# Performance work log

Hardware: AMD Instinct MI355X
Metric: run time of the kernel (lower is better)

## Reference

```python
import jax, jax.numpy as jnp
import numpy as np

SIGMA = 16.0


def setup_inputs() -> dict:
    key = jax.random.key(0)
    k1, k2, k3 = jax.random.split(key, 3)
    B, T, D = 8, 2048, 1024
    x = jax.random.normal(k1, (B, T, D), dtype=jnp.float32)
    posv = jax.random.randint(k2, (B, T), 0, 64, dtype=jnp.int32)
    posh = jax.random.randint(k3, (B, T), 0, 64, dtype=jnp.int32)
    return {"x": x, "posv": posv, "posh": posh}


def reference(x, posv, posh):
    # pos: [B, T, 2] float, as in torch.stack([posv, posh], -1).float()
    pos = jnp.stack([posv, posh], axis=-1).astype(jnp.float32)
    # pairwise squared distances: [B, T, T]
    diff = pos[:, :, None, :] - pos[:, None, :, :]
    dist_sq = jnp.sum(diff * diff, axis=-1)
    kernel = jnp.exp(-dist_sq / (2.0 * SIGMA * SIGMA))
    kernel = kernel / jnp.sum(kernel, axis=-1, keepdims=True)
    # dropout is identity in eval mode
    return jnp.einsum("bts,bsd->btd", kernel, x)
```

## Files before the change

### kernel.cpp

```cpp
#include <hip/hip_runtime.h>
#include <hip/hip_bf16.h>

#define NB 8
#define NT 2048
#define ND 1024
#define CAP 2048

typedef unsigned short ushort_t;
using short8 = __attribute__((ext_vector_type(8))) short;
using f32x4  = __attribute__((ext_vector_type(4))) float;

__device__ __forceinline__ ushort_t f2bf(float f) {
    __hip_bfloat16 h = __float2bfloat16(f);
    return *reinterpret_cast<ushort_t*>(&h);
}
__device__ __forceinline__ float bf2f(ushort_t u) {
    unsigned int v = ((unsigned int)u) << 16;
    return __int_as_float((int)v);
}


#define OFF_G2     256
#define OFF_AFH    768
#define OFF_AFL    8960
#define OFF_CNTV   17152
#define OFF_CNTH   19200
#define OFF_INVDEN 21248
#define OFF_GOFF   152320
#define OFF_TOKV   160512
#define OFF_TOKH   4354816
#define OFF_TOKV2  8549120
#define OFF_B1     12743424
#define B1_SLAB    ((size_t)64 * 64 * 1024 * 2)

__global__ __launch_bounds__(256) void k1_bucket(
    const int* __restrict__ posv, const int* __restrict__ posh,
    int* __restrict__ tokv, int* __restrict__ tokh,
    int* __restrict__ cntv, int* __restrict__ cnth,
    float* __restrict__ gbase, ushort_t* __restrict__ AfH,
    ushort_t* __restrict__ AfL)
{
    int b    = blockIdx.x >> 5;
    int blk  = blockIdx.x & 31;
    int wave = threadIdx.x >> 6;
    int lane = threadIdx.x & 63;

    if (blockIdx.x == 0) {
        if (threadIdx.x < 192) {
            int k = (int)threadIdx.x - 64;
            float v = 0.0f;
            if (k >= 0 && k < 127) {
                int r = k - 63;
                v = expf(-(float)(r * r) * (1.0f / 512.0f));
            }
            gbase[threadIdx.x] = v;
        }
#pragma unroll
        for (int p = 0; p < 16; p++) {
            int pos = (p << 8) + (int)threadIdx.x;
            int i   = pos & 7;
            int ln  = (pos >> 3) & 63;
            int ks  = (pos >> 9) & 1;
            int w   = pos >> 10;
            int q   = (w << 4) + (ln & 15);
            int k   = (ks << 5) + ((i >> 2) << 4) + ((ln >> 4) << 2) + (i & 3);
            int dlt = q - k;
            float g = expf(-(float)(dlt * dlt) * (1.0f / 512.0f));
            ushort_t hi = f2bf(g);
            AfH[pos] = hi;
            AfL[pos] = f2bf(g - bf2f(hi));
        }
    }

    int task   = blk * 4 + wave;
    int bucket = task & 63;
    int use_ph = task >> 6;
    const int* pos  = use_ph ? posh : posv;
    const int* opos = use_ph ? posv : posh;
    int* tok = (use_ph ? tokh : tokv) + ((size_t)(b * 64 + bucket)) * CAP;
    int* cnt = use_ph ? cnth : cntv;

    int vals[32];
#pragma unroll
    for (int k = 0; k < 32; k++) vals[k] = pos[b * NT + k * 64 + lane];

    unsigned long long lmask = (1ull << lane) - 1ull;
    int cursor = 0;
#pragma unroll 4
    for (int k = 0; k < 32; k++) {
        bool hit = (vals[k] == bucket);
        unsigned long long m = __ballot(hit);
        if (hit) {
            int t = k * 64 + lane;
            tok[cursor + __popcll(m & lmask)] = t | (opos[b * NT + t] << 16);
        }
        cursor += (int)__popcll(m);
    }
    if (lane == 0) cnt[b * 64 + bucket] = cursor;
}

__global__ __launch_bounds__(256) void k1b_group(
    const int* __restrict__ tokv, const int* __restrict__ cntv,
    int* __restrict__ tokv2, int4* __restrict__ goff)
{
    int bucket = blockIdx.x * 4 + (threadIdx.x >> 6);
    int lane   = threadIdx.x & 63;
    int n = cntv[bucket];
    const int* src = tokv + (size_t)bucket * CAP;
    int* dst = tokv2 + (size_t)bucket * CAP;
    unsigned long long lmask = (1ull << lane) - 1ull;

    int cnt0 = 0, cnt1 = 0, cnt2 = 0, cnt3 = 0;
    for (int base = 0; base < n; base += 64) {
        bool valid = base + lane < n;
        int pk = valid ? src[base + lane] : 0;
        int grp = (pk >> 20) & 3;
        cnt0 += (int)__popcll(__ballot(valid && grp == 0));
        cnt1 += (int)__popcll(__ballot(valid && grp == 1));
        cnt2 += (int)__popcll(__ballot(valid && grp == 2));
        cnt3 += (int)__popcll(__ballot(valid && grp == 3));
    }
    int s1 = cnt0, s2 = cnt0 + cnt1, s3 = cnt0 + cnt1 + cnt2;
    if (lane == 0) goff[bucket] = make_int4(0, s1, s2, s3);

    int c0 = 0, c1 = s1, c2 = s2, c3 = s3;
    for (int base = 0; base < n; base += 64) {
        bool valid = base + lane < n;
        int pk = valid ? src[base + lane] : 0;
        int grp = (pk >> 20) & 3;
        unsigned long long m0 = __ballot(valid && grp == 0);
        unsigned long long m1 = __ballot(valid && grp == 1);
        unsigned long long m2 = __ballot(valid && grp == 2);
        unsigned long long m3 = __ballot(valid && grp == 3);
        if (valid) {
            int p;
            if      (grp == 0) p = c0 + (int)__popcll(m0 & lmask);
            else if (grp == 1) p = c1 + (int)__popcll(m1 & lmask);
            else if (grp == 2) p = c2 + (int)__popcll(m2 & lmask);
            else               p = c3 + (int)__popcll(m3 & lmask);
            dst[p] = pk;
        }
        c0 += (int)__popcll(m0); c1 += (int)__popcll(m1);
        c2 += (int)__popcll(m2); c3 += (int)__popcll(m3);
    }
}

__global__ __launch_bounds__(256) void kden(
    const int* __restrict__ posv, const int* __restrict__ posh,
    const float* __restrict__ G2f, float* __restrict__ invden, int b0)
{
    int b   = b0 + (blockIdx.x >> 3);
    int phg = blockIdx.x & 7;
    int tid = threadIdx.x;

    __shared__ int   hist[64][64];
    __shared__ float g2s[128];
    __shared__ float tmp[64][8];

#pragma unroll
    for (int k = 0; k < 16; k++) ((int*)hist)[tid + (k << 8)] = 0;
    if (tid < 128) g2s[tid] = G2f[tid];
    __syncthreads();
#pragma unroll
    for (int k = 0; k < 8; k++) {
        int t = (k << 8) + tid;
        atomicAdd(&hist[posv[b * NT + t]][posh[b * NT + t]], 1);
    }
    __syncthreads();
#pragma unroll
    for (int c = 0; c < 2; c++) {
        int cell = (c << 8) + tid;
        int j    = cell >> 3;
        int phl  = cell & 7;
        int ph   = (phg << 3) + phl;
        float s = 0.f;
        for (int k = 0; k < 64; k++)
            s += (float)hist[j][k] * g2s[63 + k - ph];
        tmp[j][phl] = s;
    }
    __syncthreads();
#pragma unroll
    for (int c = 0; c < 2; c++) {
        int cell = (c << 8) + tid;
        int pv   = cell >> 3;
        int phl  = cell & 7;
        int ph   = (phg << 3) + phl;
        float s = 0.f;
        for (int j = 0; j < 64; j++)
            s += g2s[63 + j - pv] * tmp[j][phl];
        invden[(b * 64 + pv) * 64 + ph] = 1.0f / s;
    }
}

__device__ __forceinline__ short8 ldsBfrag(const ushort_t* rowp, int ks, int g4) {
    const ushort_t* p = rowp + (ks << 5) + g4;
    uint2 lo = *(const uint2*)(p);
    uint2 hi = *(const uint2*)(p + 16);
    uint4 pk; pk.x = lo.x; pk.y = lo.y; pk.z = hi.x; pk.w = hi.y;
    return __builtin_bit_cast(short8, pk);
}

__global__ __launch_bounds__(256) void k2_convh(
    const float* __restrict__ x,
    const int* __restrict__ tokv2, const int* __restrict__ cntv,
    const int4* __restrict__ goff,
    const ushort_t* __restrict__ AfH, const ushort_t* __restrict__ AfL,
    ushort_t* __restrict__ B1, int b0)
{
    int pv   = blockIdx.x & 63;
    int dc   = (blockIdx.x >> 6) & 15;
    int b    = b0 + (blockIdx.x >> 10);
    int tid  = threadIdx.x;
    int lane = tid & 63;
    int w    = tid >> 6;
    int d0   = dc << 6;

    __shared__ float ldsf[64 * 65];
    float    (*S)[65]   = (float(*)[65])ldsf;
    ushort_t (*S16)[68] = (ushort_t(*)[68])ldsf;

    int bucket = (b << 6) + pv;
    int n = cntv[bucket];
    const int* toks = tokv2 + (size_t)bucket * CAP;
    const float* xb = x + (((size_t)b * NT) << 10) + d0 + lane;

    int4 go = goff[bucket];
    int gs = (w == 0) ? go.x : (w == 1) ? go.y : (w == 2) ? go.z : go.w;
    int ge = (w == 3) ? n   : (w == 0) ? go.y : (w == 1) ? go.z : go.w;

    int wn0 = ge - gs; if (wn0 < 0) wn0 = 0; if (wn0 > 64) wn0 = 64;
    int m0  = wn0 > 8 ? 8 : wn0;
    int pkv = (wn0 > 0) ? toks[gs + lane] : 0;
    int pk0[8]; float xv0[8];
#pragma unroll
    for (int j = 0; j < 8; j++) pk0[j] = __builtin_amdgcn_readlane(pkv, j);
#pragma unroll
    for (int j = 0; j < 8; j++)
        if (j < m0) xv0[j] = xb[(size_t)(pk0[j] & 0xffff) << 10];

#pragma unroll
    for (int k = 0; k < 17; k++) {
        int idx = (k << 8) + tid;
        if (idx < 64 * 65) ldsf[idx] = 0.f;
    }
    __syncthreads();

#pragma unroll
    for (int j = 0; j < 8; j++)
        if (j < m0) S[lane][pk0[j] >> 16] += xv0[j];

    for (int i = 8; i < wn0; i += 8) {
        int m = wn0 - i; if (m > 8) m = 8;
        int pk[8]; float xv[8];
#pragma unroll
        for (int j = 0; j < 8; j++) pk[j] = __builtin_amdgcn_readlane(pkv, i + j);
#pragma unroll
        for (int j = 0; j < 8; j++)
            if (j < m) xv[j] = xb[(size_t)(pk[j] & 0xffff) << 10];
#pragma unroll
        for (int j = 0; j < 8; j++)
            if (j < m) S[lane][pk[j] >> 16] += xv[j];
    }
    for (int win = gs + 64; win < ge; win += 64) {
        int wn = ge - win; if (wn > 64) wn = 64;
        int pkw = toks[win + lane];
        for (int i = 0; i < wn; i += 8) {
            int m = wn - i; if (m > 8) m = 8;
            int pk[8]; float xv[8];
#pragma unroll
            for (int j = 0; j < 8; j++) pk[j] = __builtin_amdgcn_readlane(pkw, i + j);
#pragma unroll
            for (int j = 0; j < 8; j++)
                if (j < m) xv[j] = xb[(size_t)(pk[j] & 0xffff) << 10];
#pragma unroll
            for (int j = 0; j < 8; j++)
                if (j < m) S[lane][pk[j] >> 16] += xv[j];
        }
    }
    __syncthreads();

    {
        int r  = tid & 63;
        int c0 = (tid >> 6) << 4;
        float vals[16];
#pragma unroll
        for (int c = 0; c < 16; c++) vals[c] = S[r][c0 + c];
        __syncthreads();
#pragma unroll
        for (int c = 0; c < 16; c++) S16[r][c0 + c] = f2bf(vals[c]);
    }
    __syncthreads();

    short8 ahi[2], alo[2];
#pragma unroll
    for (int ks = 0; ks < 2; ks++) {
        int idx = ((((w << 1) + ks) << 6) + lane) << 3;
        ahi[ks] = *(const short8*)(AfH + idx);
        alo[ks] = *(const short8*)(AfL + idx);
    }
    int g4 = (lane >> 4) << 2;
    int qbase = (w << 4) + g4;

    f32x4 accs[4];
#pragma unroll
    for (int nt = 0; nt < 4; nt++) {
        const ushort_t* rowp = &S16[(nt << 4) + (lane & 15)][0];
        f32x4 acc = {0.f, 0.f, 0.f, 0.f};
#pragma unroll
        for (int ks = 0; ks < 2; ks++) {
            short8 bf = ldsBfrag(rowp, ks, g4);
            acc = __builtin_amdgcn_mfma_f32_16x16x32_bf16(ahi[ks], bf, acc, 0, 0, 0);
            acc = __builtin_amdgcn_mfma_f32_16x16x32_bf16(alo[ks], bf, acc, 0, 0, 0);
        }
        accs[nt] = acc;
    }
    __syncthreads();

#pragma unroll
    for (int nt = 0; nt < 4; nt++)
#pragma unroll
        for (int reg = 0; reg < 4; reg++)
            S16[qbase + reg][(nt << 4) + (lane & 15)] = f2bf(accs[nt][reg]);
    __syncthreads();

    ushort_t* B1p = B1 + (((size_t)(b - b0)) << 22) + (((size_t)pv) << 10) + d0;
#pragma unroll
    for (int pass = 0; pass < 2; pass++) {
        int row = (pass << 5) + (tid >> 3);
        int col = (tid & 7) << 3;
        uint4 v = *(const uint4*)(&S16[row][col]);
        *reinterpret_cast<uint4*>(B1p + ((size_t)row << 16) + col) = v;
    }
}

__global__ __launch_bounds__(256) void k3_convv(
    const int* __restrict__ tokh, const int* __restrict__ cnth,
    const ushort_t* __restrict__ AfH, const ushort_t* __restrict__ AfL,
    const ushort_t* __restrict__ B1, const float* __restrict__ invden,
    float* __restrict__ out, int b0)
{
    int ph   = blockIdx.x & 63;
    int dc   = (blockIdx.x >> 6) & 15;
    int b    = b0 + (blockIdx.x >> 10);
    int tid  = threadIdx.x;
    int lane = tid & 63;
    int w    = tid >> 6;
    int d0   = dc << 6;

    int n = cnth[(b << 6) + ph];
    if (n == 0) return;

    __shared__ float ldsf[64 * 65];
    ushort_t (*u16)[68] = (ushort_t(*)[68])ldsf;
    float    (*y)[65]   = (float(*)[65])ldsf;

    const ushort_t* B1b = B1 + (((size_t)(b - b0)) << 22) + (((size_t)ph) << 16)
                        + d0 + lane;
#pragma unroll
    for (int it = 0; it < 16; it++) {
        int j = (w << 4) + it;
        u16[lane][j] = B1b[(size_t)j << 10];
    }
    __syncthreads();

    short8 ahi[2], alo[2];
#pragma unroll
    for (int ks = 0; ks < 2; ks++) {
        int idx = ((((w << 1) + ks) << 6) + lane) << 3;
        ahi[ks] = *(const short8*)(AfH + idx);
        alo[ks] = *(const short8*)(AfL + idx);
    }
    int g4 = (lane >> 4) << 2;
    int qbase = (w << 4) + g4;

    f32x4 accs[4];
#pragma unroll
    for (int nt = 0; nt < 4; nt++) {
        const ushort_t* rowp = &u16[(nt << 4) + (lane & 15)][0];
        f32x4 acc = {0.f, 0.f, 0.f, 0.f};
#pragma unroll
        for (int ks = 0; ks < 2; ks++) {
            short8 bf = ldsBfrag(rowp, ks, g4);
            acc = __builtin_amdgcn_mfma_f32_16x16x32_bf16(ahi[ks], bf, acc, 0, 0, 0);
            acc = __builtin_amdgcn_mfma_f32_16x16x32_bf16(alo[ks], bf, acc, 0, 0, 0);
        }
        accs[nt] = acc;
    }
    __syncthreads();

#pragma unroll
    for (int nt = 0; nt < 4; nt++)
#pragma unroll
        for (int reg = 0; reg < 4; reg++)
            y[qbase + reg][(nt << 4) + (lane & 15)] = accs[nt][reg];
    __syncthreads();

    const int* toks = tokh + ((size_t)((b << 6) + ph)) * CAP;
    float* outb = out + (((size_t)b * NT) << 10) + d0 + lane;
    const float* ivb = invden + ((b << 6) << 6) + ph;

    int nch = (n + 3) >> 2;
    for (int c = w; c < nch; c += 4) {
        int i0 = c << 2;
        int4 M = *(const int4*)(toks + i0);
        int pk[4];
        pk[0] = __builtin_amdgcn_readfirstlane(M.x);
        pk[1] = __builtin_amdgcn_readfirstlane(M.y);
        pk[2] = __builtin_amdgcn_readfirstlane(M.z);
        pk[3] = __builtin_amdgcn_readfirstlane(M.w);
#pragma unroll
        for (int j = 0; j < 4; j++) {
            if (i0 + j < n) {
                int t   = pk[j] & 0xffff;
                int pvt = pk[j] >> 16;
                float iv = ivb[pvt << 6];
                outb[(size_t)t << 10] = y[pvt][lane] * iv;
            }
        }
    }
}

__global__ __launch_bounds__(256) void k_naive(
    const float* __restrict__ x, const int* __restrict__ posv,
    const int* __restrict__ posh, float* __restrict__ out)
{
    int t   = blockIdx.x & (NT - 1);
    int b   = blockIdx.x >> 11;
    int tid = threadIdx.x;

    __shared__ float s_w[NT];
    __shared__ float s_red[256];

    int pvt = posv[b * NT + t];
    int pht = posh[b * NT + t];

    float dsum = 0.0f;
    for (int s = tid; s < NT; s += 256) {
        int dv = pvt - posv[b * NT + s];
        int dh = pht - posh[b * NT + s];
        float w = expf(-(float)(dv * dv + dh * dh) * (1.0f / 512.0f));
        s_w[s] = w;
        dsum += w;
    }
    s_red[tid] = dsum;
    __syncthreads();
    for (int off = 128; off > 0; off >>= 1) {
        if (tid < off) s_red[tid] += s_red[tid + off];
        __syncthreads();
    }
    float inv = 1.0f / s_red[0];

    float a0 = 0.f, a1 = 0.f, a2 = 0.f, a3 = 0.f;
    for (int s = 0; s < NT; s++) {
        float w = s_w[s];
        const float* xr = x + (((size_t)(b * NT + s)) << 10);
        a0 = fmaf(w, xr[tid + 0],   a0);
        a1 = fmaf(w, xr[tid + 256], a1);
        a2 = fmaf(w, xr[tid + 512], a2);
        a3 = fmaf(w, xr[tid + 768], a3);
    }
    size_t ob = (((size_t)(b * NT + t)) << 10) + tid;
    out[ob + 0]   = a0 * inv;
    out[ob + 256] = a1 * inv;
    out[ob + 512] = a2 * inv;
    out[ob + 768] = a3 * inv;
}

extern "C" void kernel_launch(void* const* d_in, const int* in_sizes, int n_in,
                              void* d_out, int out_size, void* d_ws, size_t ws_size,
                              hipStream_t stream) {
    const float* x    = (const float*)d_in[0];
    const int*   posv = (const int*)d_in[1];
    const int*   posh = (const int*)d_in[2];
    float*       out  = (float*)d_out;

    char* ws = (char*)d_ws;
    float*    gbase  = (float*)ws;
    float*    G2f    = (float*)(ws + OFF_G2);
    ushort_t* AfH    = (ushort_t*)(ws + OFF_AFH);
    ushort_t* AfL    = (ushort_t*)(ws + OFF_AFL);
    int*      cntv   = (int*)(ws + OFF_CNTV);
    int*      cnth   = (int*)(ws + OFF_CNTH);
    float*    invden = (float*)(ws + OFF_INVDEN);
    int4*     goff   = (int4*)(ws + OFF_GOFF);
    int*      tokv   = (int*)(ws + OFF_TOKV);
    int*      tokh   = (int*)(ws + OFF_TOKH);
    int*      tokv2  = (int*)(ws + OFF_TOKV2);
    ushort_t* B1     = (ushort_t*)(ws + OFF_B1);

    const size_t needFull = (size_t)OFF_B1 + (size_t)NB * B1_SLAB;
    const size_t needLoop = (size_t)OFF_B1 + B1_SLAB;

    if (ws_size >= needFull) {
        k1_bucket<<<NB * 32, 256, 0, stream>>>(posv, posh, tokv, tokh, cntv, cnth,
                                               gbase, AfH, AfL);
        k1b_group<<<NB * 16, 256, 0, stream>>>(tokv, cntv, tokv2, goff);
        kden<<<NB * 8, 256, 0, stream>>>(posv, posh, G2f, invden, 0);
        k2_convh<<<NB * 1024, 256, 0, stream>>>(x, tokv2, cntv, goff, AfH, AfL, B1, 0);
        k3_convv<<<NB * 1024, 256, 0, stream>>>(tokh, cnth, AfH, AfL, B1, invden, out, 0);
    } else if (ws_size >= needLoop) {
        k1_bucket<<<NB * 32, 256, 0, stream>>>(posv, posh, tokv, tokh, cntv, cnth,
                                               gbase, AfH, AfL);
        k1b_group<<<NB * 16, 256, 0, stream>>>(tokv, cntv, tokv2, goff);
        for (int b = 0; b < NB; b++) {
            kden<<<8, 256, 0, stream>>>(posv, posh, G2f, invden, b);
            k2_convh<<<1024, 256, 0, stream>>>(x, tokv2, cntv, goff, AfH, AfL, B1, b);
            k3_convv<<<1024, 256, 0, stream>>>(tokh, cnth, AfH, AfL, B1, invden, out, b);
        }
    } else {
        k_naive<<<NB * NT, 256, 0, stream>>>(x, posv, posh, out);
    }
}
```

Before: 78.20 us.

## Fuse bucketing, grouping and denominator kernels into one launch

Merges the separate grouping pass into the bucketing kernel, so v-buckets are written already sorted into the four groups straight from registers. The denominator computation now runs as extra blocks of the same launch and computes its Gaussian table inline. This removes two kernel launches and the tokv round-trip through global memory. The cost is that every bucket wave loads both position arrays and makes two ballot passes.

```diff
diff --git a/kernel.cpp b/kernel.cpp
--- a/kernel.cpp
+++ b/kernel.cpp
@@ -33,13 +33,69 @@
 #define OFF_B1     12743424
 #define B1_SLAB    ((size_t)64 * 64 * 1024 * 2)
 
+__device__ __forceinline__ void kden_body(
+    int kb, const int* __restrict__ posv, const int* __restrict__ posh,
+    float* __restrict__ invden, int b0)
+{
+    int b   = b0 + (kb >> 3);
+    int phg = kb & 7;
+    int tid = threadIdx.x;
+
+    __shared__ int   hist[64][64];
+    __shared__ float g2s[128];
+    __shared__ float tmp[64][8];
+
+#pragma unroll
+    for (int k = 0; k < 16; k++) ((int*)hist)[tid + (k << 8)] = 0;
+    if (tid < 128) {
+        int k = tid, r = k - 63;
+        g2s[tid] = (k < 127) ? expf(-(float)(r * r) * (1.0f / 512.0f)) : 0.0f;
+    }
+    __syncthreads();
+#pragma unroll
+    for (int k = 0; k < 8; k++) {
+        int t = (k << 8) + tid;
+        atomicAdd(&hist[posv[b * NT + t]][posh[b * NT + t]], 1);
+    }
+    __syncthreads();
+#pragma unroll
+    for (int c = 0; c < 2; c++) {
+        int cell = (c << 8) + tid;
+        int j    = cell >> 3;
+        int phl  = cell & 7;
+        int ph   = (phg << 3) + phl;
+        float s = 0.f;
+        for (int k = 0; k < 64; k++)
+            s += (float)hist[j][k] * g2s[63 + k - ph];
+        tmp[j][phl] = s;
+    }
+    __syncthreads();
+#pragma unroll
+    for (int c = 0; c < 2; c++) {
+        int cell = (c << 8) + tid;
+        int pv   = cell >> 3;
+        int phl  = cell & 7;
+        int ph   = (phg << 3) + phl;
+        float s = 0.f;
+        for (int j = 0; j < 64; j++)
+            s += g2s[63 + j - pv] * tmp[j][phl];
+        invden[(b * 64 + pv) * 64 + ph] = 1.0f / s;
+    }
+}
+
 __global__ __launch_bounds__(256) void k1_bucket(
     const int* __restrict__ posv, const int* __restrict__ posh,
-    int* __restrict__ tokv, int* __restrict__ tokh,
+    int* __restrict__ tokv2, int4* __restrict__ goff,
+    int* __restrict__ tokh,
     int* __restrict__ cntv, int* __restrict__ cnth,
     float* __restrict__ gbase, ushort_t* __restrict__ AfH,
-    ushort_t* __restrict__ AfL)
+    ushort_t* __restrict__ AfL, float* __restrict__ invden, int nbkt)
 {
+    if ((int)blockIdx.x >= nbkt) {
+        kden_body((int)blockIdx.x - nbkt, posv, posh, invden, 0);
+        return;
+    }
+
     int b    = blockIdx.x >> 5;
     int blk  = blockIdx.x & 31;
     int wave = threadIdx.x >> 6;
@@ -75,121 +131,76 @@
     int task   = blk * 4 + wave;
     int bucket = task & 63;
     int use_ph = task >> 6;
-    const int* pos  = use_ph ? posh : posv;
-    const int* opos = use_ph ? posv : posh;
-    int* tok = (use_ph ? tokh : tokv) + ((size_t)(b * 64 + bucket)) * CAP;
-    int* cnt = use_ph ? cnth : cntv;
-
-    int vals[32];
-#pragma unroll
-    for (int k = 0; k < 32; k++) vals[k] = pos[b * NT + k * 64 + lane];
+    int bkt    = b * 64 + bucket;
+
+    int comb[32];
+#pragma unroll
+    for (int k = 0; k < 32; k++) {
+        int t = k * 64 + lane;
+        comb[k] = posv[b * NT + t] | (posh[b * NT + t] << 16);
+    }
 
     unsigned long long lmask = (1ull << lane) - 1ull;
-    int cursor = 0;
+
+    if (use_ph == 0) {
+        int* dst = tokv2 + (size_t)bkt * CAP;
+        int cg0 = 0, cg1 = 0, cg2 = 0, cg3 = 0;
 #pragma unroll 4
-    for (int k = 0; k < 32; k++) {
-        bool hit = (vals[k] == bucket);
-        unsigned long long m = __ballot(hit);
-        if (hit) {
-            int t = k * 64 + lane;
-            tok[cursor + __popcll(m & lmask)] = t | (opos[b * NT + t] << 16);
-        }
-        cursor += (int)__popcll(m);
-    }
-    if (lane == 0) cnt[b * 64 + bucket] = cursor;
-}
-
-__global__ __launch_bounds__(256) void k1b_group(
-    const int* __restrict__ tokv, const int* __restrict__ cntv,
-    int* __restrict__ tokv2, int4* __restrict__ goff)
-{
-    int bucket = blockIdx.x * 4 + (threadIdx.x >> 6);
-    int lane   = threadIdx.x & 63;
-    int n = cntv[bucket];
-    const int* src = tokv + (size_t)bucket * CAP;
-    int* dst = tokv2 + (size_t)bucket * CAP;
-    unsigned long long lmask = (1ull << lane) - 1ull;
-
-    int cnt0 = 0, cnt1 = 0, cnt2 = 0, cnt3 = 0;
-    for (int base = 0; base < n; base += 64) {
-        bool valid = base + lane < n;
-        int pk = valid ? src[base + lane] : 0;
-        int grp = (pk >> 20) & 3;
-        cnt0 += (int)__popcll(__ballot(valid && grp == 0));
-        cnt1 += (int)__popcll(__ballot(valid && grp == 1));
-        cnt2 += (int)__popcll(__ballot(valid && grp == 2));
-        cnt3 += (int)__popcll(__ballot(valid && grp == 3));
-    }
-    int s1 = cnt0, s2 = cnt0 + cnt1, s3 = cnt0 + cnt1 + cnt2;
-    if (lane == 0) goff[bucket] = make_int4(0, s1, s2, s3);
-
-    int c0 = 0, c1 = s1, c2 = s2, c3 = s3;
-    for (int base = 0; base < n; base += 64) {
-        bool valid = base + lane < n;
-        int pk = valid ? src[base + lane] : 0;
-        int grp = (pk >> 20) & 3;
-        unsigned long long m0 = __ballot(valid && grp == 0);
-        unsigned long long m1 = __ballot(valid && grp == 1);
-        unsigned long long m2 = __ballot(valid && grp == 2);
-        unsigned long long m3 = __ballot(valid && grp == 3);
-        if (valid) {
-            int p;
-            if      (grp == 0) p = c0 + (int)__popcll(m0 & lmask);
-            else if (grp == 1) p = c1 + (int)__popcll(m1 & lmask);
-            else if (grp == 2) p = c2 + (int)__popcll(m2 & lmask);
-            else               p = c3 + (int)__popcll(m3 & lmask);
-            dst[p] = pk;
-        }
-        c0 += (int)__popcll(m0); c1 += (int)__popcll(m1);
-        c2 += (int)__popcll(m2); c3 += (int)__popcll(m3);
+        for (int k = 0; k < 32; k++) {
+            bool hit = (comb[k] & 0xffff) == bucket;
+            int grp = (comb[k] >> 20) & 3;
+            cg0 += (int)__popcll(__ballot(hit && grp == 0));
+            cg1 += (int)__popcll(__ballot(hit && grp == 1));
+            cg2 += (int)__popcll(__ballot(hit && grp == 2));
+            cg3 += (int)__popcll(__ballot(hit && grp == 3));
+        }
+        int s1 = cg0, s2 = cg0 + cg1, s3 = cg0 + cg1 + cg2;
+        int tot = s3 + cg3;
+        if (lane == 0) {
+            goff[bkt] = make_int4(0, s1, s2, s3);
+            cntv[bkt] = tot;
+        }
+        int c0 = 0, c1 = s1, c2 = s2, c3 = s3;
+#pragma unroll 4
+        for (int k = 0; k < 32; k++) {
+            bool hit = (comb[k] & 0xffff) == bucket;
+            int grp = (comb[k] >> 20) & 3;
+            unsigned long long m0 = __ballot(hit && grp == 0);
+            unsigned long long m1 = __ballot(hit && grp == 1);
+            unsigned long long m2 = __ballot(hit && grp == 2);
+            unsigned long long m3 = __ballot(hit && grp == 3);
+            if (hit) {
+                int p;
+                if      (grp == 0) p = c0 + (int)__popcll(m0 & lmask);
+                else if (grp == 1) p = c1 + (int)__popcll(m1 & lmask);
+                else if (grp == 2) p = c2 + (int)__popcll(m2 & lmask);
+                else               p = c3 + (int)__popcll(m3 & lmask);
+                dst[p] = (k * 64 + lane) | (comb[k] & 0xffff0000);
+            }
+            c0 += (int)__popcll(m0); c1 += (int)__popcll(m1);
+            c2 += (int)__popcll(m2); c3 += (int)__popcll(m3);
+        }
+    } else {
+        int* dst = tokh + (size_t)bkt * CAP;
+        int cursor = 0;
+#pragma unroll 4
+        for (int k = 0; k < 32; k++) {
+            bool hit = ((comb[k] >> 16) == bucket);
+            unsigned long long m = __ballot(hit);
+            if (hit)
+                dst[cursor + __popcll(m & lmask)] =
+                    (k * 64 + lane) | ((comb[k] & 0xffff) << 16);
+            cursor += (int)__popcll(m);
+        }
+        if (lane == 0) cnth[bkt] = cursor;
     }
 }
 
 __global__ __launch_bounds__(256) void kden(
     const int* __restrict__ posv, const int* __restrict__ posh,
-    const float* __restrict__ G2f, float* __restrict__ invden, int b0)
+    float* __restrict__ invden, int b0)
 {
-    int b   = b0 + (blockIdx.x >> 3);
-    int phg = blockIdx.x & 7;
-    int tid = threadIdx.x;
-
-    __shared__ int   hist[64][64];
-    __shared__ float g2s[128];
-    __shared__ float tmp[64][8];
-
-#pragma unroll
-    for (int k = 0; k < 16; k++) ((int*)hist)[tid + (k << 8)] = 0;
-    if (tid < 128) g2s[tid] = G2f[tid];
-    __syncthreads();
-#pragma unroll
-    for (int k = 0; k < 8; k++) {
-        int t = (k << 8) + tid;
-        atomicAdd(&hist[posv[b * NT + t]][posh[b * NT + t]], 1);
-    }
-    __syncthreads();
-#pragma unroll
-    for (int c = 0; c < 2; c++) {
-        int cell = (c << 8) + tid;
-        int j    = cell >> 3;
-        int phl  = cell & 7;
-        int ph   = (phg << 3) + phl;
-        float s = 0.f;
-        for (int k = 0; k < 64; k++)
-            s += (float)hist[j][k] * g2s[63 + k - ph];
-        tmp[j][phl] = s;
-    }
-    __syncthreads();
-#pragma unroll
-    for (int c = 0; c < 2; c++) {
-        int cell = (c << 8) + tid;
-        int pv   = cell >> 3;
-        int phl  = cell & 7;
-        int ph   = (phg << 3) + phl;
-        float s = 0.f;
-        for (int j = 0; j < 64; j++)
-            s += g2s[63 + j - pv] * tmp[j][phl];
-        invden[(b * 64 + pv) * 64 + ph] = 1.0f / s;
-    }
+    kden_body((int)blockIdx.x, posv, posh, invden, b0);
 }
 
 __device__ __forceinline__ short8 ldsBfrag(const ushort_t* rowp, int ks, int g4) {
@@ -305,14 +316,14 @@
 #pragma unroll
     for (int nt = 0; nt < 4; nt++) {
         const ushort_t* rowp = &S16[(nt << 4) + (lane & 15)][0];
-        f32x4 acc = {0.f, 0.f, 0.f, 0.f};
+        f32x4 a = {0.f, 0.f, 0.f, 0.f};
 #pragma unroll
         for (int ks = 0; ks < 2; ks++) {
             short8 bf = ldsBfrag(rowp, ks, g4);
-            acc = __builtin_amdgcn_mfma_f32_16x16x32_bf16(ahi[ks], bf, acc, 0, 0, 0);
-            acc = __builtin_amdgcn_mfma_f32_16x16x32_bf16(alo[ks], bf, acc, 0, 0, 0);
-        }
-        accs[nt] = acc;
+            a = __builtin_amdgcn_mfma_f32_16x16x32_bf16(ahi[ks], bf, a, 0, 0, 0);
+            a = __builtin_amdgcn_mfma_f32_16x16x32_bf16(alo[ks], bf, a, 0, 0, 0);
+        }
+        accs[nt] = a;
     }
     __syncthreads();
 
@@ -377,14 +388,14 @@
 #pragma unroll
     for (int nt = 0; nt < 4; nt++) {
         const ushort_t* rowp = &u16[(nt << 4) + (lane & 15)][0];
-        f32x4 acc = {0.f, 0.f, 0.f, 0.f};
+        f32x4 a = {0.f, 0.f, 0.f, 0.f};
 #pragma unroll
         for (int ks = 0; ks < 2; ks++) {
             short8 bf = ldsBfrag(rowp, ks, g4);
-            acc = __builtin_amdgcn_mfma_f32_16x16x32_bf16(ahi[ks], bf, acc, 0, 0, 0);
-            acc = __builtin_amdgcn_mfma_f32_16x16x32_bf16(alo[ks], bf, acc, 0, 0, 0);
-        }
-        accs[nt] = acc;
+            a = __builtin_amdgcn_mfma_f32_16x16x32_bf16(ahi[ks], bf, a, 0, 0, 0);
+            a = __builtin_amdgcn_mfma_f32_16x16x32_bf16(alo[ks], bf, a, 0, 0, 0);
+        }
+        accs[nt] = a;
     }
     __syncthreads();
 
@@ -476,14 +487,12 @@
 
     char* ws = (char*)d_ws;
     float*    gbase  = (float*)ws;
-    float*    G2f    = (float*)(ws + OFF_G2);
     ushort_t* AfH    = (ushort_t*)(ws + OFF_AFH);
     ushort_t* AfL    = (ushort_t*)(ws + OFF_AFL);
     int*      cntv   = (int*)(ws + OFF_CNTV);
     int*      cnth   = (int*)(ws + OFF_CNTH);
     float*    invden = (float*)(ws + OFF_INVDEN);
     int4*     goff   = (int4*)(ws + OFF_GOFF);
-    int*      tokv   = (int*)(ws + OFF_TOKV);
     int*      tokh   = (int*)(ws + OFF_TOKH);
     int*      tokv2  = (int*)(ws + OFF_TOKV2);
     ushort_t* B1     = (ushort_t*)(ws + OFF_B1);
@@ -492,18 +501,17 @@
     const size_t needLoop = (size_t)OFF_B1 + B1_SLAB;
 
     if (ws_size >= needFull) {
-        k1_bucket<<<NB * 32, 256, 0, stream>>>(posv, posh, tokv, tokh, cntv, cnth,
-                                               gbase, AfH, AfL);
-        k1b_group<<<NB * 16, 256, 0, stream>>>(tokv, cntv, tokv2, goff);
-        kden<<<NB * 8, 256, 0, stream>>>(posv, posh, G2f, invden, 0);
+        k1_bucket<<<NB * 32 + NB * 8, 256, 0, stream>>>(
+            posv, posh, tokv2, goff, tokh, cntv, cnth, gbase, AfH, AfL,
+            invden, NB * 32);
         k2_convh<<<NB * 1024, 256, 0, stream>>>(x, tokv2, cntv, goff, AfH, AfL, B1, 0);
         k3_convv<<<NB * 1024, 256, 0, stream>>>(tokh, cnth, AfH, AfL, B1, invden, out, 0);
     } else if (ws_size >= needLoop) {
-        k1_bucket<<<NB * 32, 256, 0, stream>>>(posv, posh, tokv, tokh, cntv, cnth,
-                                               gbase, AfH, AfL);
-        k1b_group<<<NB * 16, 256, 0, stream>>>(tokv, cntv, tokv2, goff);
+        k1_bucket<<<NB * 32, 256, 0, stream>>>(
+            posv, posh, tokv2, goff, tokh, cntv, cnth, gbase, AfH, AfL,
+            invden, NB * 32);
         for (int b = 0; b < NB; b++) {
-            kden<<<8, 256, 0, stream>>>(posv, posh, G2f, invden, b);
+            kden<<<8, 256, 0, stream>>>(posv, posh, invden, b);
             k2_convh<<<1024, 256, 0, stream>>>(x, tokv2, cntv, goff, AfH, AfL, B1, b);
             k3_convv<<<1024, 256, 0, stream>>>(tokh, cnth, AfH, AfL, B1, invden, out, b);
         }
```

New measurement: 73.16 us. 6.4% less time.
